# Kernel tuning notes

Hardware: AMD Instinct MI355X
Metric: run time of the kernel (lower is better)

Reference implementation:

```python
import jax, jax.numpy as jnp
import numpy as np

NUM_NODES = 262144        # 1024 graphs x 256 nodes
NODES_PER_GRAPH = 256
NUM_GRAPHS = NUM_NODES // NODES_PER_GRAPH
NUM_EDGES = 2097152       # avg degree 8
NUM_FEATURES = 9
NUM_STATIONS = 8


def setup_inputs() -> dict:
    key = jax.random.key(0)
    ks = jax.random.split(key, 12)
    # edges constrained within each graph so batched-graph semantics hold
    src_local = jax.random.randint(ks[0], (NUM_EDGES,), 0, NODES_PER_GRAPH)
    dst_local = jax.random.randint(ks[1], (NUM_EDGES,), 0, NODES_PER_GRAPH)
    graph_of_edge = jax.random.randint(ks[2], (NUM_EDGES,), 0, NUM_GRAPHS)
    offset = graph_of_edge * NODES_PER_GRAPH
    edge_index = jnp.stack([src_local + offset, dst_local + offset]).astype(jnp.int64)
    station_ids = jnp.array([0, 37, 73, 110, 146, 183, 219, 255], dtype=jnp.int64)
    s = lambda k, shape, fan_in: jax.random.normal(k, shape, jnp.float32) / np.sqrt(fan_in)
    return {
        "x": jax.random.normal(ks[3], (NUM_NODES, NUM_FEATURES), jnp.float32),
        "edge_index": edge_index,
        "station_ids": station_ids,
        "W1": s(ks[4], (NUM_FEATURES, 32), NUM_FEATURES),
        "b1": jnp.zeros((32,), jnp.float32),
        "W2": s(ks[5], (32, 64), 32),
        "b2": jnp.zeros((64,), jnp.float32),
        "fc1_W": s(ks[6], (128, 64), 128),
        "fc1_b": jnp.zeros((64,), jnp.float32),
        "fc2_W": s(ks[7], (64, 1), 64),
        "fc2_b": jnp.zeros((1,), jnp.float32),
    }


def _gcn_conv(x, W, b, src, dst, n_nodes):
    """PyG GCNConv: add self-loops, symmetric normalization, linear first."""
    h = x @ W                                              # [N, C_out]
    # degree includes the self-loop (+1), counted on target nodes
    deg = jnp.zeros((n_nodes,), h.dtype).at[dst].add(1.0) + 1.0
    dinv = jax.lax.rsqrt(deg)                              # deg >= 1, safe
    norm = dinv[src] * dinv[dst]                           # [E]
    out = jnp.zeros_like(h).at[dst].add(norm[:, None] * h[src])
    out = out + (dinv * dinv)[:, None] * h                 # self-loop term
    return out + b


def reference(x, edge_index, station_ids, W1, b1, W2, b2, fc1_W, fc1_b, fc2_W, fc2_b):
    n = x.shape[0]
    src, dst = edge_index[0], edge_index[1]
    h = jax.nn.relu(_gcn_conv(x, W1, b1, src, dst, n))     # [N, 32]
    h = jax.nn.relu(_gcn_conv(h, W2, b2, src, dst, n))     # [N, 64]
    # global mean pool per graph (batch = node_idx // NODES_PER_GRAPH)
    batch = jnp.arange(n) // NODES_PER_GRAPH
    sums = jax.ops.segment_sum(h, batch, num_segments=NUM_GRAPHS)
    counts = jax.ops.segment_sum(jnp.ones((n,), h.dtype), batch, num_segments=NUM_GRAPHS)
    global_ctx = sums / counts[:, None]                    # [B, 64]
    # per-station gather-MLP, vectorized over stations
    idx = jnp.arange(NUM_GRAPHS)[:, None] * NODES_PER_GRAPH + station_ids[None, :]  # [B, S]
    station_emb = h[idx]                                   # [B, S, 64]
    ctx = jnp.broadcast_to(global_ctx[:, None, :], station_emb.shape)
    combined = jnp.concatenate([station_emb, ctx], axis=-1)  # [B, S, 128]
    q = jax.nn.relu(combined @ fc1_W + fc1_b) @ fc2_W + fc2_b  # [B, S, 1]
    return q[..., 0]                                       # [B, S]
```

## Files before the change

### kernel.cpp

```cpp
#include <hip/hip_runtime.h>
#include <hip/hip_bf16.h>


#define NNODES 262144
#define NPG 256
#define NGRAPHS 1024
#define NEDGES 2097152
#define NFEAT 9
#define ECAP2 2560
#define T_EDGES 8192
#define NTILES (NEDGES / T_EDGES)
#define TPB 1024
#define NBLK 256

typedef __hip_bfloat16 bf16;
typedef short short8 __attribute__((ext_vector_type(8)));
typedef float f32x4 __attribute__((ext_vector_type(4)));

__device__ __forceinline__ float bfbits(unsigned short u) { return __uint_as_float(((unsigned)u) << 16); }
__device__ __forceinline__ unsigned short f2bbits(float v) { bf16 b = __float2bfloat16(v); return *(unsigned short*)&b; }


__global__ void __launch_bounds__(1024) k_hist(const int* __restrict__ dst,
                                               int* __restrict__ hist) {
    __shared__ int cnt[NGRAPHS];
    int t = threadIdx.x;
    cnt[t] = 0;
    __syncthreads();
    const int4* d4 = (const int4*)(dst + blockIdx.x * T_EDGES);
#pragma unroll
    for (int k = 0; k < T_EDGES / 4096; ++k) {
        int4 dv = d4[k * 1024 + t];
        atomicAdd(&cnt[dv.x >> 8], 1);
        atomicAdd(&cnt[dv.y >> 8], 1);
        atomicAdd(&cnt[dv.z >> 8], 1);
        atomicAdd(&cnt[dv.w >> 8], 1);
    }
    __syncthreads();
    hist[blockIdx.x * NGRAPHS + t] = cnt[t];
}

__global__ void __launch_bounds__(256) k_scan(int* __restrict__ hist,
                                              int* __restrict__ gcnt) {
    __shared__ int wsum[4];
    int g = blockIdx.x;
    int t = threadIdx.x;
    int lane = t & 63, wv = t >> 6;
    int v = hist[t * NGRAPHS + g];
    int inc = v;
    for (int off = 1; off < 64; off <<= 1) {
        int y = __shfl_up(inc, off);
        if (lane >= off) inc += y;
    }
    if (lane == 63) wsum[wv] = inc;
    __syncthreads();
    int wpre = 0;
#pragma unroll
    for (int w = 0; w < 3; ++w) if (w < wv) wpre += wsum[w];
    int exc = wpre + inc - v;
    hist[t * NGRAPHS + g] = exc;
    if (t == 255) gcnt[g * 16] = exc + v;
}

__global__ void __launch_bounds__(1024) k_scatter(const int* __restrict__ src,
                                                  const int* __restrict__ dst,
                                                  const int* __restrict__ hist,
                                                  unsigned short* __restrict__ gout) {
    __shared__ unsigned short sg[T_EDGES];
    __shared__ unsigned short pay[T_EDGES];
    __shared__ unsigned short spay[T_EDGES];
    __shared__ unsigned short ssg[T_EDGES];
    __shared__ int cnt[NGRAPHS];
    __shared__ int lbase[NGRAPHS];
    __shared__ int gb[NGRAPHS];
    __shared__ int wsum[16];
    int t = threadIdx.x;
    int lane = t & 63, wv = t >> 6;
    int base = blockIdx.x * T_EDGES;
    cnt[t] = 0;
    gb[t] = hist[blockIdx.x * NGRAPHS + t];
    __syncthreads();
    const int4* s4 = (const int4*)(src + base);
    const int4* d4 = (const int4*)(dst + base);
#pragma unroll
    for (int k = 0; k < T_EDGES / 4096; ++k) {
        int idx = k * 1024 + t;
        int4 dv = d4[idx];
        int4 sv = s4[idx];
        int i0 = idx * 4;
        sg[i0]     = (unsigned short)(dv.x >> 8);
        sg[i0 + 1] = (unsigned short)(dv.y >> 8);
        sg[i0 + 2] = (unsigned short)(dv.z >> 8);
        sg[i0 + 3] = (unsigned short)(dv.w >> 8);
        pay[i0]     = (unsigned short)(((dv.x & 255) << 8) | (sv.x & 255));
        pay[i0 + 1] = (unsigned short)(((dv.y & 255) << 8) | (sv.y & 255));
        pay[i0 + 2] = (unsigned short)(((dv.z & 255) << 8) | (sv.z & 255));
        pay[i0 + 3] = (unsigned short)(((dv.w & 255) << 8) | (sv.w & 255));
        atomicAdd(&cnt[dv.x >> 8], 1);
        atomicAdd(&cnt[dv.y >> 8], 1);
        atomicAdd(&cnt[dv.z >> 8], 1);
        atomicAdd(&cnt[dv.w >> 8], 1);
    }
    __syncthreads();
    int c = cnt[t];
    int inc = c;
    for (int off = 1; off < 64; off <<= 1) {
        int y = __shfl_up(inc, off);
        if (lane >= off) inc += y;
    }
    if (lane == 63) wsum[wv] = inc;
    __syncthreads();
    int wpre = 0;
    for (int w = 0; w < wv; ++w) wpre += wsum[w];
    lbase[t] = wpre + inc - c;
    cnt[t] = 0;
    __syncthreads();
#pragma unroll
    for (int k = 0; k < T_EDGES / 1024; ++k) {
        int i = k * 1024 + t;
        int g = sg[i];
        int p = lbase[g] + atomicAdd(&cnt[g], 1);
        spay[p] = pay[i];
        ssg[p] = (unsigned short)g;
    }
    __syncthreads();
#pragma unroll
    for (int k = 0; k < T_EDGES / 1024; ++k) {
        int p = k * 1024 + t;
        int g = ssg[p];
        int off = gb[g] + (p - lbase[g]);
        if (off < ECAP2) gout[(size_t)g * ECAP2 + off] = spay[p];
    }
}


__global__ void __launch_bounds__(TPB) k_fused(
    const float* __restrict__ x, const int* __restrict__ station_ids,
    const float* __restrict__ W1, const float* __restrict__ b1,
    const float* __restrict__ W2, const float* __restrict__ b2,
    const float* __restrict__ fc1W, const float* __restrict__ fc1b,
    const float* __restrict__ fc2W, const float* __restrict__ fc2b,
    const int* __restrict__ gcnt, const unsigned short* __restrict__ gedges,
    float* __restrict__ out) {

    __shared__ __align__(16) unsigned char Ms[65536];
    __shared__ __align__(16) unsigned char BufA[17024];
    __shared__ __align__(16) unsigned char BufB[17024];
    __shared__ __align__(16) unsigned char BufC[19456];
    __shared__ __align__(16) unsigned short fc1s16[8192];
    __shared__ __align__(16) unsigned short W2Ts[64 * 40];
    __shared__ float W1s[288];
    __shared__ float dinvs[256];
    __shared__ unsigned short Rl[260];
    __shared__ unsigned char El[ECAP2];
    __shared__ unsigned int sru[512];
    __shared__ float sts[512];
    __shared__ float meanf[64];
    __shared__ float poolf[64];
    __shared__ unsigned char stmap[256];
    __shared__ float b1s[32], b2s[64], fc1bs[64], fc2ws[64];
    __shared__ int stids[8];
    __shared__ float fc2bv;

    int t = threadIdx.x;
    int lane = t & 63, wvid = t >> 6;
    int m = lane & 15, quad = lane >> 4;
    int wr = wvid >> 1, wn = wvid & 1;

    float* xsf = (float*)BufC;
    unsigned short* EPa = (unsigned short*)(BufC + 9216);
    unsigned short* G1T = (unsigned short*)BufA;
    unsigned short* H1T = (unsigned short*)BufB;
    unsigned short* S2 = (unsigned short*)BufC;

    for (int i = t; i < NFEAT * 32; i += TPB) W1s[i] = W1[i];
    for (int i = t; i < 2048; i += TPB)
        W2Ts[(i >> 5) * 40 + (i & 31)] = f2bbits(W2[(i & 31) * 64 + (i >> 5)]);
    for (int i = t; i < 8192; i += TPB) fc1s16[i] = f2bbits(fc1W[i]);
    if (t < 32) b1s[t] = b1[t];
    if (t < 64) { b2s[t] = b2[t]; fc1bs[t] = fc1b[t]; fc2ws[t] = fc2W[t]; }
    if (t < 8) stids[t] = station_ids[t];
    if (t == 0) fc2bv = fc2b[0];
    if (t < 256) stmap[t] = 255;
    __syncthreads();
    if (t < 8) stmap[stids[t] & 255] = (unsigned char)t;

    for (int g = blockIdx.x; g < NGRAPHS; g += NBLK) {
        int nbase = g * NPG;

        int ecnt = min(gcnt[g * 16], ECAP2);
        {
            const uint4* gev = (const uint4*)(gedges + (size_t)g * ECAP2);
            uint4* epv = (uint4*)EPa;
            for (int i = t; i < ECAP2 / 8; i += TPB) epv[i] = gev[i];
        }
        const float* xg = x + (size_t)nbase * NFEAT;
        for (int i = t; i < NPG * NFEAT; i += TPB) xsf[i] = xg[i];
        if (t < 64) poolf[t] = 0.f;
        if (t < 256) sru[t] = 0u;
        {
            uint4* mz = (uint4*)Ms;
            uint4 z = {0u, 0u, 0u, 0u};
            for (int i = t; i < 4096; i += TPB) mz[i] = z;
        }
        __syncthreads();

        for (int i = t; i < ecnt; i += TPB) atomicAdd(&sru[EPa[i] >> 8], 1u);
        __syncthreads();

        if (wvid == 0) {
            int b0 = sru[lane * 4], b1v = sru[lane * 4 + 1], b2v = sru[lane * 4 + 2], b3 = sru[lane * 4 + 3];
            int s = b0 + b1v + b2v + b3;
            int inc = s;
            for (int off = 1; off < 64; off <<= 1) {
                int y = __shfl_up(inc, off);
                if (lane >= off) inc += y;
            }
            int run = inc - s;
            Rl[lane * 4] = (unsigned short)run; sru[256 + lane * 4] = run;
            dinvs[lane * 4] = rsqrtf((float)(b0 + 1)); run += b0;
            Rl[lane * 4 + 1] = (unsigned short)run; sru[257 + lane * 4] = run;
            dinvs[lane * 4 + 1] = rsqrtf((float)(b1v + 1)); run += b1v;
            Rl[lane * 4 + 2] = (unsigned short)run; sru[258 + lane * 4] = run;
            dinvs[lane * 4 + 2] = rsqrtf((float)(b2v + 1)); run += b2v;
            Rl[lane * 4 + 3] = (unsigned short)run; sru[259 + lane * 4] = run;
            dinvs[lane * 4 + 3] = rsqrtf((float)(b3 + 1));
            if (lane == 63) Rl[256] = (unsigned short)inc;
        }
        __syncthreads();

        for (int i = t; i < ecnt; i += TPB) {
            unsigned short v = EPa[i];
            unsigned p = atomicAdd(&sru[256 + (v >> 8)], 1u);
            if (p < ECAP2) El[p] = (unsigned char)(v & 255);
        }
        __syncthreads();

        if (t < 512) {
            int dl = t >> 2, q = t & 3;
            int d = dl;
            float did = dinvs[d];
            if ((d >> 6) == q)
                *(unsigned short*)(Ms + dl * 512 + (((d >> 3) ^ (d & 15)) * 16) + (d & 7) * 2)
                    = f2bbits(did * did);
            int r0 = Rl[d], r1 = Rl[d + 1];
            for (int e = r0; e < r1; ++e) {
                int s = El[e];
                if ((s >> 6) == q) {
                    unsigned short* p =
                        (unsigned short*)(Ms + dl * 512 + (((s >> 3) ^ (d & 15)) * 16) + (s & 7) * 2);
                    *p = f2bbits(bfbits(*p) + did * dinvs[s]);
                }
            }
        } else {
            int tt = t - 512;
            int n = tt >> 1, half = tt & 1;
            float xv[NFEAT];
#pragma unroll
            for (int k = 0; k < NFEAT; k++) xv[k] = xsf[n * NFEAT + k];
            int c0 = half * 16;
#pragma unroll 4
            for (int ci = 0; ci < 16; ci++) {
                int c = c0 + ci;
                float acc = 0.f;
#pragma unroll
                for (int k = 0; k < NFEAT; k++) acc += xv[k] * W1s[k * 32 + c];
                G1T[c * 266 + n] = f2bbits(acc);
            }
        }
        __syncthreads();

        {
            f32x4 acc = {};
            for (int kt = 0; kt < 8; ++kt) {
                short8 af = *(const short8*)(Ms + (wr * 16 + m) * 512 + (((kt * 4 + quad) ^ m) * 16));
                short8 bf = *(const short8*)(BufA + (size_t)(wn * 16 + m) * 532 + kt * 64 + quad * 16);
                acc = __builtin_amdgcn_mfma_f32_16x16x32_bf16(af, bf, acc, 0, 0, 0);
            }
            int ch = wn * 16 + m;
            float bb = b1s[ch];
#pragma unroll
            for (int r = 0; r < 4; ++r) {
                int node = wr * 16 + quad * 4 + r;
                H1T[ch * 266 + node] = f2bbits(fmaxf(acc[r] + bb, 0.f));
            }
        }
        __syncthreads();

        {
            uint4* mz = (uint4*)Ms;
            uint4 z = {0u, 0u, 0u, 0u};
            for (int i = t; i < 4096; i += TPB) mz[i] = z;
        }
        __syncthreads();
        {
            int dl = t >> 3, q = t & 7;
            int d = 128 + dl;
            float did = dinvs[d];
            int sd = d & 255;
            if ((sd >> 5) == q) {
                *(unsigned short*)(Ms + dl * 512 + (((sd >> 3) ^ (d & 15)) * 16) + (sd & 7) * 2)
                    = f2bbits(did * did);
            }
            int r0 = Rl[d], r1 = Rl[d + 1];
            for (int e = r0; e < r1; ++e) {
                int s = El[e];
                if ((s >> 5) == q) {
                    unsigned short* p =
                        (unsigned short*)(Ms + dl * 512 + (((s >> 3) ^ (d & 15)) * 16) + (s & 7) * 2);
                    *p = f2bbits(bfbits(*p) + did * dinvs[s]);
                }
            }
        }
        __syncthreads();

        {
            f32x4 acc = {};
            for (int kt = 0; kt < 8; ++kt) {
                short8 af = *(const short8*)(Ms + (wr * 16 + m) * 512 + (((kt * 4 + quad) ^ m) * 16));
                short8 bf = *(const short8*)(BufA + (size_t)(wn * 16 + m) * 532 + kt * 64 + quad * 16);
                acc = __builtin_amdgcn_mfma_f32_16x16x32_bf16(af, bf, acc, 0, 0, 0);
            }
            int ch = wn * 16 + m;
            float bb = b1s[ch];
#pragma unroll
            for (int r = 0; r < 4; ++r) {
                int node = 128 + wr * 16 + quad * 4 + r;
                H1T[ch * 266 + node] = f2bbits(fmaxf(acc[r] + bb, 0.f));
            }
        }
        __syncthreads();

        {
            f32x4 acc = {};
            for (int kt = 0; kt < 8; ++kt) {
                short8 af = *(const short8*)(Ms + (wr * 16 + m) * 512 + (((kt * 4 + quad) ^ m) * 16));
                short8 bf = *(const short8*)(BufB + (size_t)(wn * 16 + m) * 532 + kt * 64 + quad * 16);
                acc = __builtin_amdgcn_mfma_f32_16x16x32_bf16(af, bf, acc, 0, 0, 0);
            }
            int ch = wn * 16 + m;
#pragma unroll
            for (int r = 0; r < 4; ++r) {
                int node = 128 + wr * 16 + quad * 4 + r;
                S2[node * 38 + ch] = f2bbits(acc[r]);
            }
        }
        __syncthreads();

        {
            uint4* mz = (uint4*)Ms;
            uint4 z = {0u, 0u, 0u, 0u};
            for (int i = t; i < 4096; i += TPB) mz[i] = z;
        }
        __syncthreads();
        {
            int dl = t >> 3, q = t & 7;
            int d = dl;
            float did = dinvs[d];
            if ((d >> 5) == q)
                *(unsigned short*)(Ms + dl * 512 + (((d >> 3) ^ (d & 15)) * 16) + (d & 7) * 2)
                    = f2bbits(did * did);
            int r0 = Rl[d], r1 = Rl[d + 1];
            for (int e = r0; e < r1; ++e) {
                int s = El[e];
                if ((s >> 5) == q) {
                    unsigned short* p =
                        (unsigned short*)(Ms + dl * 512 + (((s >> 3) ^ (d & 15)) * 16) + (s & 7) * 2);
                    *p = f2bbits(bfbits(*p) + did * dinvs[s]);
                }
            }
        }
        __syncthreads();

        {
            f32x4 acc = {};
            for (int kt = 0; kt < 8; ++kt) {
                short8 af = *(const short8*)(Ms + (wr * 16 + m) * 512 + (((kt * 4 + quad) ^ m) * 16));
                short8 bf = *(const short8*)(BufB + (size_t)(wn * 16 + m) * 532 + kt * 64 + quad * 16);
                acc = __builtin_amdgcn_mfma_f32_16x16x32_bf16(af, bf, acc, 0, 0, 0);
            }
            int ch = wn * 16 + m;
#pragma unroll
            for (int r = 0; r < 4; ++r) {
                int node = wr * 16 + quad * 4 + r;
                S2[node * 38 + ch] = f2bbits(acc[r]);
            }
        }
        __syncthreads();

        {
            int mt = wvid;
            short8 af = *(const short8*)(BufC + (size_t)(mt * 16 + m) * 76 + quad * 16);
#pragma unroll
            for (int ni = 0; ni < 4; ++ni) {
                short8 bf = *(const short8*)((const unsigned char*)W2Ts + (size_t)(ni * 16 + m) * 80 + quad * 16);
                f32x4 c = {};
                c = __builtin_amdgcn_mfma_f32_16x16x32_bf16(af, bf, c, 0, 0, 0);
                int ch = ni * 16 + m;
                float bb = b2s[ch];
                float hv[4];
                float p = 0.f;
#pragma unroll
                for (int r = 0; r < 4; ++r) { hv[r] = fmaxf(c[r] + bb, 0.f); p += hv[r]; }
                p += __shfl_down(p, 32);
                p += __shfl_down(p, 16);
                if (quad == 0) atomicAdd(&poolf[ch], p);
#pragma unroll
                for (int r = 0; r < 4; ++r) {
                    int node = mt * 16 + quad * 4 + r;
                    int si = stmap[node];
                    if (si != 255) sts[si * 64 + ch] = hv[r];
                }
            }
        }
        __syncthreads();

        if (t < 64) meanf[t] = poolf[t] * (1.0f / 256.0f);
        __syncthreads();

        if (wvid < 8) {
            int l = lane;
            int si = wvid;
            const float* st = sts + si * 64;
            float acc = 0.f;
#pragma unroll 8
            for (int k = 0; k < 64; k++) acc += st[k] * bfbits(fc1s16[k * 64 + l]);
#pragma unroll 8
            for (int k = 0; k < 64; k++) acc += meanf[k] * bfbits(fc1s16[(64 + k) * 64 + l]);
            float a = fmaxf(acc + fc1bs[l], 0.f) * fc2ws[l];
            for (int off = 32; off > 0; off >>= 1) a += __shfl_down(a, off);
            if (l == 0) out[g * 8 + si] = a + fc2bv;
        }
        __syncthreads();
    }
}


extern "C" void kernel_launch(void* const* d_in, const int* in_sizes, int n_in,
                              void* d_out, int out_size, void* d_ws, size_t ws_size,
                              hipStream_t stream) {
    const float* x = (const float*)d_in[0];
    const int* ei = (const int*)d_in[1];
    const int* station_ids = (const int*)d_in[2];
    const float* W1 = (const float*)d_in[3];
    const float* b1 = (const float*)d_in[4];
    const float* W2 = (const float*)d_in[5];
    const float* bias2 = (const float*)d_in[6];
    const float* fc1W = (const float*)d_in[7];
    const float* fc1b = (const float*)d_in[8];
    const float* fc2W = (const float*)d_in[9];
    const float* fc2b = (const float*)d_in[10];
    float* out = (float*)d_out;
    (void)in_sizes; (void)n_in; (void)out_size; (void)ws_size;

    char* ws = (char*)d_ws;
    int* gcnt = (int*)ws;
    unsigned short* gout = (unsigned short*)(ws + 0x10000);
    int* hist = (int*)(ws + 0x510000);

    const int* esrc = ei;
    const int* edst = ei + NEDGES;

    k_hist<<<NTILES, 1024, 0, stream>>>(edst, hist);
    k_scan<<<NGRAPHS, 256, 0, stream>>>(hist, gcnt);
    k_scatter<<<NTILES, 1024, 0, stream>>>(esrc, edst, hist, gout);
    k_fused<<<NBLK, TPB, 0, stream>>>(x, station_ids, W1, b1, W2, bias2,
                                      fc1W, fc1b, fc2W, fc2b, gcnt, gout, out);
}
```

Baseline: 188.0 us.

## Build full 256x256 adjacency once per graph and restructure GCN stages around it

Enlarges the shared adjacency buffer so the full normalized 256x256 matrix is built once per graph and reused by both GCN layers, where before it was rebuilt in two halves per layer with repeated zeroing and extra barriers. Each wave now computes 16 nodes against all 32 channels with swizzled layouts, reads x straight from global, and keeps W2 fragments in registers. The final fc1 MLP moves to a single-wave MFMA, with fc1 weights reloaded and converted into spare adjacency space each graph. The cost is much larger LDS use and per-graph global reloads of fc1W.

```diff
diff --git a/kernel.cpp b/kernel.cpp
--- a/kernel.cpp
+++ b/kernel.cpp
@@ -143,20 +143,17 @@
     const int* __restrict__ gcnt, const unsigned short* __restrict__ gedges,
     float* __restrict__ out) {
 
-    __shared__ __align__(16) unsigned char Ms[65536];
-    __shared__ __align__(16) unsigned char BufA[17024];
-    __shared__ __align__(16) unsigned char BufB[17024];
-    __shared__ __align__(16) unsigned char BufC[19456];
-    __shared__ __align__(16) unsigned short fc1s16[8192];
-    __shared__ __align__(16) unsigned short W2Ts[64 * 40];
+    __shared__ __align__(16) unsigned char Ms[131072];
+    __shared__ __align__(16) unsigned char Buf[16384];
+    __shared__ __align__(16) unsigned short EPa[ECAP2];
+    __shared__ unsigned char El[ECAP2];
+    __shared__ unsigned int sru[256];
+    __shared__ unsigned short Rl[260];
+    __shared__ float dinvs[256];
     __shared__ float W1s[288];
-    __shared__ float dinvs[256];
-    __shared__ unsigned short Rl[260];
-    __shared__ unsigned char El[ECAP2];
-    __shared__ unsigned int sru[512];
     __shared__ float sts[512];
+    __shared__ float poolf[64];
     __shared__ float meanf[64];
-    __shared__ float poolf[64];
     __shared__ unsigned char stmap[256];
     __shared__ float b1s[32], b2s[64], fc1bs[64], fc2ws[64];
     __shared__ int stids[8];
@@ -165,28 +162,23 @@
     int t = threadIdx.x;
     int lane = t & 63, wvid = t >> 6;
     int m = lane & 15, quad = lane >> 4;
-    int wr = wvid >> 1, wn = wvid & 1;
-
-    float* xsf = (float*)BufC;
-    unsigned short* EPa = (unsigned short*)(BufC + 9216);
-    unsigned short* G1T = (unsigned short*)BufA;
-    unsigned short* H1T = (unsigned short*)BufB;
-    unsigned short* S2 = (unsigned short*)BufC;
 
     for (int i = t; i < NFEAT * 32; i += TPB) W1s[i] = W1[i];
-    for (int i = t; i < 2048; i += TPB)
-        W2Ts[(i >> 5) * 40 + (i & 31)] = f2bbits(W2[(i & 31) * 64 + (i >> 5)]);
-    for (int i = t; i < 8192; i += TPB) fc1s16[i] = f2bbits(fc1W[i]);
     if (t < 32) b1s[t] = b1[t];
     if (t < 64) { b2s[t] = b2[t]; fc1bs[t] = fc1b[t]; fc2ws[t] = fc2W[t]; }
     if (t < 8) stids[t] = station_ids[t];
     if (t == 0) fc2bv = fc2b[0];
     if (t < 256) stmap[t] = 255;
+    short8 w2f[4];
+#pragma unroll
+    for (int ni = 0; ni < 4; ++ni)
+#pragma unroll
+        for (int j = 0; j < 8; ++j)
+            w2f[ni][j] = (short)f2bbits(W2[(quad * 8 + j) * 64 + ni * 16 + m]);
     __syncthreads();
     if (t < 8) stmap[stids[t] & 255] = (unsigned char)t;
 
     for (int g = blockIdx.x; g < NGRAPHS; g += NBLK) {
-        int nbase = g * NPG;
 
         int ecnt = min(gcnt[g * 16], ECAP2);
         {
@@ -194,208 +186,138 @@
             uint4* epv = (uint4*)EPa;
             for (int i = t; i < ECAP2 / 8; i += TPB) epv[i] = gev[i];
         }
-        const float* xg = x + (size_t)nbase * NFEAT;
-        for (int i = t; i < NPG * NFEAT; i += TPB) xsf[i] = xg[i];
-        if (t < 64) poolf[t] = 0.f;
         if (t < 256) sru[t] = 0u;
-        {
-            uint4* mz = (uint4*)Ms;
-            uint4 z = {0u, 0u, 0u, 0u};
-            for (int i = t; i < 4096; i += TPB) mz[i] = z;
-        }
+        if (t >= 256 && t < 320) poolf[t - 256] = 0.f;
         __syncthreads();
 
         for (int i = t; i < ecnt; i += TPB) atomicAdd(&sru[EPa[i] >> 8], 1u);
         __syncthreads();
 
         if (wvid == 0) {
-            int b0 = sru[lane * 4], b1v = sru[lane * 4 + 1], b2v = sru[lane * 4 + 2], b3 = sru[lane * 4 + 3];
+            int b0 = sru[lane * 4], b1v = sru[lane * 4 + 1];
+            int b2v = sru[lane * 4 + 2], b3 = sru[lane * 4 + 3];
             int s = b0 + b1v + b2v + b3;
             int inc = s;
             for (int off = 1; off < 64; off <<= 1) {
                 int y = __shfl_up(inc, off);
                 if (lane >= off) inc += y;
             }
-            int run = inc - s;
-            Rl[lane * 4] = (unsigned short)run; sru[256 + lane * 4] = run;
-            dinvs[lane * 4] = rsqrtf((float)(b0 + 1)); run += b0;
-            Rl[lane * 4 + 1] = (unsigned short)run; sru[257 + lane * 4] = run;
-            dinvs[lane * 4 + 1] = rsqrtf((float)(b1v + 1)); run += b1v;
-            Rl[lane * 4 + 2] = (unsigned short)run; sru[258 + lane * 4] = run;
-            dinvs[lane * 4 + 2] = rsqrtf((float)(b2v + 1)); run += b2v;
-            Rl[lane * 4 + 3] = (unsigned short)run; sru[259 + lane * 4] = run;
-            dinvs[lane * 4 + 3] = rsqrtf((float)(b3 + 1));
+            int r0 = inc - s;
+            int r1 = r0 + b0, r2 = r1 + b1v, r3 = r2 + b2v;
+            Rl[lane * 4] = (unsigned short)r0;     dinvs[lane * 4] = rsqrtf((float)(b0 + 1));
+            Rl[lane * 4 + 1] = (unsigned short)r1; dinvs[lane * 4 + 1] = rsqrtf((float)(b1v + 1));
+            Rl[lane * 4 + 2] = (unsigned short)r2; dinvs[lane * 4 + 2] = rsqrtf((float)(b2v + 1));
+            Rl[lane * 4 + 3] = (unsigned short)r3; dinvs[lane * 4 + 3] = rsqrtf((float)(b3 + 1));
+            sru[lane * 4] = r0; sru[lane * 4 + 1] = r1;
+            sru[lane * 4 + 2] = r2; sru[lane * 4 + 3] = r3;
             if (lane == 63) Rl[256] = (unsigned short)inc;
         }
         __syncthreads();
 
         for (int i = t; i < ecnt; i += TPB) {
             unsigned short v = EPa[i];
-            unsigned p = atomicAdd(&sru[256 + (v >> 8)], 1u);
+            unsigned p = atomicAdd(&sru[v >> 8], 1u);
             if (p < ECAP2) El[p] = (unsigned char)(v & 255);
         }
         __syncthreads();
 
         if (t < 512) {
-            int dl = t >> 2, q = t & 3;
-            int d = dl;
+            int d = t >> 1, q = t & 1;
+            uint4* mz = (uint4*)(Ms + d * 512 + q * 256);
+            uint4 z = {0u, 0u, 0u, 0u};
+#pragma unroll
+            for (int i = 0; i < 16; ++i) mz[i] = z;
             float did = dinvs[d];
-            if ((d >> 6) == q)
-                *(unsigned short*)(Ms + dl * 512 + (((d >> 3) ^ (d & 15)) * 16) + (d & 7) * 2)
+            if ((d >> 7) == q)
+                *(unsigned short*)(Ms + d * 512 + (((d >> 3) ^ (d & 15)) * 16) + (d & 7) * 2)
                     = f2bbits(did * did);
             int r0 = Rl[d], r1 = Rl[d + 1];
             for (int e = r0; e < r1; ++e) {
                 int s = El[e];
-                if ((s >> 6) == q) {
+                if ((s >> 7) == q) {
                     unsigned short* p =
-                        (unsigned short*)(Ms + dl * 512 + (((s >> 3) ^ (d & 15)) * 16) + (s & 7) * 2);
+                        (unsigned short*)(Ms + d * 512 + (((s >> 3) ^ (d & 15)) * 16) + (s & 7) * 2);
                     *p = f2bbits(bfbits(*p) + did * dinvs[s]);
                 }
             }
         } else {
             int tt = t - 512;
             int n = tt >> 1, half = tt & 1;
+            const float* xr = x + (size_t)(g * NPG + n) * NFEAT;
             float xv[NFEAT];
 #pragma unroll
-            for (int k = 0; k < NFEAT; k++) xv[k] = xsf[n * NFEAT + k];
+            for (int k = 0; k < NFEAT; ++k) xv[k] = xr[k];
             int c0 = half * 16;
 #pragma unroll 4
-            for (int ci = 0; ci < 16; ci++) {
+            for (int ci = 0; ci < 16; ++ci) {
                 int c = c0 + ci;
                 float acc = 0.f;
 #pragma unroll
-                for (int k = 0; k < NFEAT; k++) acc += xv[k] * W1s[k * 32 + c];
-                G1T[c * 266 + n] = f2bbits(acc);
+                for (int k = 0; k < NFEAT; ++k) acc += xv[k] * W1s[k * 32 + c];
+                *(unsigned short*)(Buf + c * 512 + (((n >> 3) ^ (c & 15)) * 16) + (n & 7) * 2)
+                    = f2bbits(acc);
+            }
+        }
+        __syncthreads();
+
+        f32x4 acc1[2] = {};
+        for (int kt = 0; kt < 8; ++kt) {
+            short8 af = *(const short8*)(Ms + (size_t)(wvid * 16 + m) * 512 + (((kt * 4 + quad) ^ m) * 16));
+            short8 bf0 = *(const short8*)(Buf + (size_t)m * 512 + (((kt * 4 + quad) ^ m) * 16));
+            short8 bf1 = *(const short8*)(Buf + (size_t)(16 + m) * 512 + (((kt * 4 + quad) ^ m) * 16));
+            acc1[0] = __builtin_amdgcn_mfma_f32_16x16x32_bf16(af, bf0, acc1[0], 0, 0, 0);
+            acc1[1] = __builtin_amdgcn_mfma_f32_16x16x32_bf16(af, bf1, acc1[1], 0, 0, 0);
+        }
+        __syncthreads();
+
+#pragma unroll
+        for (int ct = 0; ct < 2; ++ct) {
+            int ch = ct * 16 + m;
+            float bb = b1s[ch];
+#pragma unroll
+            for (int r = 0; r < 4; ++r) {
+                int node = wvid * 16 + quad * 4 + r;
+                *(unsigned short*)(Buf + (size_t)ch * 512 + (((node >> 3) ^ (ch & 15)) * 16) + (node & 7) * 2)
+                    = f2bbits(fmaxf(acc1[ct][r] + bb, 0.f));
             }
         }
         __syncthreads();
 
         {
-            f32x4 acc = {};
+            f32x4 a2[2] = {};
             for (int kt = 0; kt < 8; ++kt) {
-                short8 af = *(const short8*)(Ms + (wr * 16 + m) * 512 + (((kt * 4 + quad) ^ m) * 16));
-                short8 bf = *(const short8*)(BufA + (size_t)(wn * 16 + m) * 532 + kt * 64 + quad * 16);
-                acc = __builtin_amdgcn_mfma_f32_16x16x32_bf16(af, bf, acc, 0, 0, 0);
-            }
-            int ch = wn * 16 + m;
-            float bb = b1s[ch];
-#pragma unroll
-            for (int r = 0; r < 4; ++r) {
-                int node = wr * 16 + quad * 4 + r;
-                H1T[ch * 266 + node] = f2bbits(fmaxf(acc[r] + bb, 0.f));
-            }
-        }
-        __syncthreads();
-
-        {
-            uint4* mz = (uint4*)Ms;
-            uint4 z = {0u, 0u, 0u, 0u};
-            for (int i = t; i < 4096; i += TPB) mz[i] = z;
-        }
-        __syncthreads();
-        {
-            int dl = t >> 3, q = t & 7;
-            int d = 128 + dl;
-            float did = dinvs[d];
-            int sd = d & 255;
-            if ((sd >> 5) == q) {
-                *(unsigned short*)(Ms + dl * 512 + (((sd >> 3) ^ (d & 15)) * 16) + (sd & 7) * 2)
-                    = f2bbits(did * did);
-            }
-            int r0 = Rl[d], r1 = Rl[d + 1];
-            for (int e = r0; e < r1; ++e) {
-                int s = El[e];
-                if ((s >> 5) == q) {
-                    unsigned short* p =
-                        (unsigned short*)(Ms + dl * 512 + (((s >> 3) ^ (d & 15)) * 16) + (s & 7) * 2);
-                    *p = f2bbits(bfbits(*p) + did * dinvs[s]);
+                short8 af = *(const short8*)(Ms + (size_t)(wvid * 16 + m) * 512 + (((kt * 4 + quad) ^ m) * 16));
+                short8 bf0 = *(const short8*)(Buf + (size_t)m * 512 + (((kt * 4 + quad) ^ m) * 16));
+                short8 bf1 = *(const short8*)(Buf + (size_t)(16 + m) * 512 + (((kt * 4 + quad) ^ m) * 16));
+                a2[0] = __builtin_amdgcn_mfma_f32_16x16x32_bf16(af, bf0, a2[0], 0, 0, 0);
+                a2[1] = __builtin_amdgcn_mfma_f32_16x16x32_bf16(af, bf1, a2[1], 0, 0, 0);
+            }
+#pragma unroll
+            for (int ct = 0; ct < 2; ++ct) {
+                int ch = ct * 16 + m;
+                int c8 = ch >> 3;
+#pragma unroll
+                for (int r = 0; r < 4; ++r) {
+                    int node = wvid * 16 + quad * 4 + r;
+                    *(unsigned short*)(Ms + (size_t)node * 512 + ((c8 ^ (node & 3)) * 16) + (ch & 7) * 2)
+                        = f2bbits(a2[ct][r]);
                 }
             }
         }
         __syncthreads();
 
-        {
-            f32x4 acc = {};
-            for (int kt = 0; kt < 8; ++kt) {
-                short8 af = *(const short8*)(Ms + (wr * 16 + m) * 512 + (((kt * 4 + quad) ^ m) * 16));
-                short8 bf = *(const short8*)(BufA + (size_t)(wn * 16 + m) * 532 + kt * 64 + quad * 16);
-                acc = __builtin_amdgcn_mfma_f32_16x16x32_bf16(af, bf, acc, 0, 0, 0);
-            }
-            int ch = wn * 16 + m;
-            float bb = b1s[ch];
-#pragma unroll
-            for (int r = 0; r < 4; ++r) {
-                int node = 128 + wr * 16 + quad * 4 + r;
-                H1T[ch * 266 + node] = f2bbits(fmaxf(acc[r] + bb, 0.f));
-            }
-        }
-        __syncthreads();
-
-        {
-            f32x4 acc = {};
-            for (int kt = 0; kt < 8; ++kt) {
-                short8 af = *(const short8*)(Ms + (wr * 16 + m) * 512 + (((kt * 4 + quad) ^ m) * 16));
-                short8 bf = *(const short8*)(BufB + (size_t)(wn * 16 + m) * 532 + kt * 64 + quad * 16);
-                acc = __builtin_amdgcn_mfma_f32_16x16x32_bf16(af, bf, acc, 0, 0, 0);
-            }
-            int ch = wn * 16 + m;
-#pragma unroll
-            for (int r = 0; r < 4; ++r) {
-                int node = 128 + wr * 16 + quad * 4 + r;
-                S2[node * 38 + ch] = f2bbits(acc[r]);
-            }
-        }
-        __syncthreads();
-
-        {
-            uint4* mz = (uint4*)Ms;
-            uint4 z = {0u, 0u, 0u, 0u};
-            for (int i = t; i < 4096; i += TPB) mz[i] = z;
-        }
-        __syncthreads();
-        {
-            int dl = t >> 3, q = t & 7;
-            int d = dl;
-            float did = dinvs[d];
-            if ((d >> 5) == q)
-                *(unsigned short*)(Ms + dl * 512 + (((d >> 3) ^ (d & 15)) * 16) + (d & 7) * 2)
-                    = f2bbits(did * did);
-            int r0 = Rl[d], r1 = Rl[d + 1];
-            for (int e = r0; e < r1; ++e) {
-                int s = El[e];
-                if ((s >> 5) == q) {
-                    unsigned short* p =
-                        (unsigned short*)(Ms + dl * 512 + (((s >> 3) ^ (d & 15)) * 16) + (s & 7) * 2);
-                    *p = f2bbits(bfbits(*p) + did * dinvs[s]);
-                }
-            }
-        }
-        __syncthreads();
-
-        {
-            f32x4 acc = {};
-            for (int kt = 0; kt < 8; ++kt) {
-                short8 af = *(const short8*)(Ms + (wr * 16 + m) * 512 + (((kt * 4 + quad) ^ m) * 16));
-                short8 bf = *(const short8*)(BufB + (size_t)(wn * 16 + m) * 532 + kt * 64 + quad * 16);
-                acc = __builtin_amdgcn_mfma_f32_16x16x32_bf16(af, bf, acc, 0, 0, 0);
-            }
-            int ch = wn * 16 + m;
-#pragma unroll
-            for (int r = 0; r < 4; ++r) {
-                int node = wr * 16 + quad * 4 + r;
-                S2[node * 38 + ch] = f2bbits(acc[r]);
-            }
-        }
-        __syncthreads();
-
+        for (int i = t; i < 8192; i += TPB) {
+            int k = i >> 6, c2 = i & 63;
+            *(unsigned short*)(Ms + (size_t)c2 * 512 + 256 + (((k >> 3) ^ (c2 & 15)) * 16) + (k & 7) * 2)
+                = f2bbits(fc1W[i]);
+        }
         {
             int mt = wvid;
-            short8 af = *(const short8*)(BufC + (size_t)(mt * 16 + m) * 76 + quad * 16);
+            short8 af = *(const short8*)(Ms + (size_t)(mt * 16 + m) * 512 + ((quad ^ (m & 3)) * 16));
 #pragma unroll
             for (int ni = 0; ni < 4; ++ni) {
-                short8 bf = *(const short8*)((const unsigned char*)W2Ts + (size_t)(ni * 16 + m) * 80 + quad * 16);
                 f32x4 c = {};
-                c = __builtin_amdgcn_mfma_f32_16x16x32_bf16(af, bf, c, 0, 0, 0);
+                c = __builtin_amdgcn_mfma_f32_16x16x32_bf16(af, w2f[ni], c, 0, 0, 0);
                 int ch = ni * 16 + m;
                 float bb = b2s[ch];
                 float hv[4];
@@ -418,18 +340,39 @@
         if (t < 64) meanf[t] = poolf[t] * (1.0f / 256.0f);
         __syncthreads();
 
-        if (wvid < 8) {
-            int l = lane;
-            int si = wvid;
-            const float* st = sts + si * 64;
-            float acc = 0.f;
-#pragma unroll 8
-            for (int k = 0; k < 64; k++) acc += st[k] * bfbits(fc1s16[k * 64 + l]);
-#pragma unroll 8
-            for (int k = 0; k < 64; k++) acc += meanf[k] * bfbits(fc1s16[(64 + k) * 64 + l]);
-            float a = fmaxf(acc + fc1bs[l], 0.f) * fc2ws[l];
-            for (int off = 32; off > 0; off >>= 1) a += __shfl_down(a, off);
-            if (l == 0) out[g * 8 + si] = a + fc2bv;
+        if (wvid == 0) {
+            short8 af4[4];
+#pragma unroll
+            for (int kt = 0; kt < 4; ++kt) {
+#pragma unroll
+                for (int j = 0; j < 8; ++j) {
+                    int k = kt * 32 + quad * 8 + j;
+                    float v = (m < 8) ? (k < 64 ? sts[m * 64 + k] : meanf[k - 64]) : 0.f;
+                    af4[kt][j] = (short)f2bbits(v);
+                }
+            }
+            f32x4 cc[4];
+#pragma unroll
+            for (int ni = 0; ni < 4; ++ni) {
+                f32x4 c = {};
+#pragma unroll
+                for (int kt = 0; kt < 4; ++kt) {
+                    short8 bf = *(const short8*)(Ms + (size_t)(ni * 16 + m) * 512 + 256 + (((kt * 4 + quad) ^ m) * 16));
+                    c = __builtin_amdgcn_mfma_f32_16x16x32_bf16(af4[kt], bf, c, 0, 0, 0);
+                }
+                cc[ni] = c;
+            }
+#pragma unroll
+            for (int r = 0; r < 4; ++r) {
+                float a = 0.f;
+#pragma unroll
+                for (int ni = 0; ni < 4; ++ni)
+                    a += fmaxf(cc[ni][r] + fc1bs[ni * 16 + m], 0.f) * fc2ws[ni * 16 + m];
+#pragma unroll
+                for (int off = 1; off < 16; off <<= 1) a += __shfl_xor(a, off);
+                int st = quad * 4 + r;
+                if (m == 0 && st < 8) out[g * 8 + st] = a + fc2bv;
+            }
         }
         __syncthreads();
     }
```

After: 172.8 us. 1.09x faster.
